# Kernel tuning notes

Measured on AMD Instinct MI355X. Metric: run time of the kernel, lower is better.

The kernel has to match this reference:

```python
import jax, jax.numpy as jnp
import numpy as np

N_HEADS = 8
HEAD_DIM = 32
MODEL_DIM = N_HEADS * HEAD_DIM  # 256
IN_DIM = 256
N_MEM = 4
B, H, W = 4, 64, 64
SCALE = HEAD_DIM ** -0.5


def setup_inputs() -> dict:
    key = jax.random.key(0)
    ks = jax.random.split(key, 6)
    x = jax.random.normal(ks[0], (B, IN_DIM, H, W), dtype=jnp.float32)
    w_qkv = jax.random.normal(ks[1], (MODEL_DIM * 3, IN_DIM), dtype=jnp.float32) * 0.02
    b_qkv = jnp.zeros((MODEL_DIM * 3,), dtype=jnp.float32)
    mem_kv = jax.random.normal(ks[2], (2, N_HEADS, N_MEM, HEAD_DIM), dtype=jnp.float32)
    w_out = jax.random.normal(ks[3], (IN_DIM, MODEL_DIM), dtype=jnp.float32) * 0.02
    b_out = jnp.zeros((IN_DIM,), dtype=jnp.float32)
    return {"x": x, "w_qkv": w_qkv, "b_qkv": b_qkv, "mem_kv": mem_kv,
            "w_out": w_out, "b_out": b_out}


def reference(x, w_qkv, b_qkv, mem_kv, w_out, b_out):
    b, c, h, w = x.shape
    n = h * w
    # 1x1 conv == per-pixel matmul over channels
    qkv = jnp.einsum('bchw,oc->bohw', x, w_qkv) + b_qkv[None, :, None, None]
    q, k, v = jnp.split(qkv, 3, axis=1)
    # 'b (n d) h w -> b n (h w) d'
    def to_heads(t):
        return t.reshape(b, N_HEADS, HEAD_DIM, n).transpose(0, 1, 3, 2)
    q, k, v = to_heads(q), to_heads(k), to_heads(v)
    # prepend memory kv tokens: [b, n_heads, N_MEM + n, d]
    mk = jnp.broadcast_to(mem_kv[0][None], (b, N_HEADS, N_MEM, HEAD_DIM))
    mv = jnp.broadcast_to(mem_kv[1][None], (b, N_HEADS, N_MEM, HEAD_DIM))
    k = jnp.concatenate([mk, k], axis=-2)
    v = jnp.concatenate([mv, v], axis=-2)
    # scaled dot-product attention (dropout prob = 0 -> identity)
    sim = jnp.einsum('bnid,bnsd->bnis', q, k) * SCALE
    attn = jax.nn.softmax(sim, axis=-1)
    out = jnp.einsum('bnis,bnsd->bnid', attn, v)
    # 'b n (h w) d -> b (n d) h w'
    out = out.transpose(0, 1, 3, 2).reshape(b, MODEL_DIM, h, w)
    out = jnp.einsum('bchw,oc->bohw', out, w_out) + b_out[None, :, None, None]
    return out
```

## Files before the change

### kernel.cpp

```cpp
#include <hip/hip_runtime.h>
#include <stdint.h>


#define DEV static __device__ __forceinline__

typedef short s16x8 __attribute__((ext_vector_type(8)));
typedef float f32x4 __attribute__((ext_vector_type(4)));
typedef unsigned short ushort_t;

DEV unsigned short f2b(float f) {
  return (unsigned short)((__float_as_uint(f) + 0x8000u) >> 16);
}
DEV unsigned pkf2b(float a, float b) {
  return __builtin_amdgcn_perm(__float_as_uint(b) + 0x8000u,
                               __float_as_uint(a) + 0x8000u, 0x07060302u);
}

DEV void gld16(const void* g, void* l) {
  __builtin_amdgcn_global_load_lds(
      (const __attribute__((address_space(1))) unsigned int*)g,
      (__attribute__((address_space(3))) unsigned int*)l, 16, 0, 0);
}

__global__ __launch_bounds__(256) void pack_x(const float* __restrict__ x,
                                              ushort_t* __restrict__ xT) {
  __shared__ float t[64][65];
  const int b = blockIdx.z, cb = blockIdx.y, pb = blockIdx.x;
  const int tid = threadIdx.x;
#pragma unroll
  for (int i = 0; i < 16; ++i) {
    int idx = i * 256 + tid;
    int cl = idx >> 6, pl = idx & 63;
    t[cl][pl] = x[((size_t)(b * 256 + cb * 64 + cl)) * 4096 + pb * 64 + pl];
  }
  __syncthreads();
#pragma unroll
  for (int i = 0; i < 8; ++i) {
    int idx = i * 256 + tid;
    int pl = idx >> 5, c2 = idx & 31;
    unsigned w = pkf2b(t[c2 * 2][pl], t[c2 * 2 + 1][pl]);
    *(unsigned*)(xT + ((size_t)(b * 4096 + pb * 64 + pl)) * 256 + cb * 64 + c2 * 2) = w;
  }
}

__global__ __launch_bounds__(256) void pack_small(
    const float* __restrict__ wqkv, const float* __restrict__ wout,
    const float* __restrict__ memkv, ushort_t* __restrict__ wqkvb,
    ushort_t* __restrict__ woutb, ushort_t* __restrict__ Kb,
    ushort_t* __restrict__ Vt) {
  int idx = blockIdx.x * 256 + threadIdx.x;
  if (idx < 196608) { wqkvb[idx] = f2b(wqkv[idx]); return; }
  idx -= 196608;
  if (idx < 65536) { woutb[idx] = f2b(wout[idx]); return; }
  idx -= 65536;
  if (idx < 131072) {
    int bh = idx >> 12, r = idx & 4095;
    int row = 4096 + (r >> 5), d = r & 31, h = bh & 7;
    float v = (row < 4100) ? memkv[h * 128 + (row - 4096) * 32 + d] : 0.f;
    Kb[((size_t)(bh * 4224 + row)) * 32 + d] = f2b(v);
    return;
  }
  idx -= 131072;
  {
    int bh = idx >> 12, r = idx & 4095;
    int d = r >> 7, col = 4096 + (r & 127), h = bh & 7;
    float v = (col < 4100) ? memkv[1024 + h * 128 + (col - 4096) * 32 + d] : 0.f;
    Vt[((size_t)(bh * 32 + d)) * 4224 + col] = f2b(v);
  }
}

__global__ __launch_bounds__(256) void qkv_gemm(
    const ushort_t* __restrict__ W, const ushort_t* __restrict__ X,
    const float* __restrict__ bias, ushort_t* __restrict__ Qb,
    ushort_t* __restrict__ Kb, ushort_t* __restrict__ Vt) {
  __shared__ ushort_t sA[128 * 32];
  __shared__ ushort_t sB[128 * 32];
  const int tid = threadIdx.x, wave = tid >> 6, lane = tid & 63;
  const int quad = lane >> 4, ln = lane & 15;
  const int b = blockIdx.z, my = blockIdx.y, nx = blockIdx.x;
  const int o0 = my * 128, p0 = nx * 128;
  const int wr = wave >> 1, wc = wave & 1;
  const ushort_t* Xb = X + (size_t)b * 4096 * 256;
  f32x4 acc[4][4];
#pragma unroll
  for (int i = 0; i < 4; ++i)
#pragma unroll
    for (int j = 0; j < 4; ++j) acc[i][j] = {0.f, 0.f, 0.f, 0.f};

  const int srow_in = lane >> 2, sgs = lane & 3;
  for (int kt = 0; kt < 8; ++kt) {
    const int k0 = kt * 32;
#pragma unroll
    for (int i2 = 0; i2 < 2; ++i2) {
      const int i = wave * 2 + i2;
      const int row = i * 16 + srow_in;
      const int gg = sgs ^ ((row >> 1) & 3);
      gld16(W + (size_t)(o0 + row) * 256 + k0 + gg * 8, sA + i * 512);
      gld16(Xb + (size_t)(p0 + row) * 256 + k0 + gg * 8, sB + i * 512);
    }
    __syncthreads();
    s16x8 af[4], bfv[4];
#pragma unroll
    for (int mt = 0; mt < 4; ++mt) {
      const int row = wr * 64 + mt * 16 + ln;
      af[mt] = *(const s16x8*)(sA + row * 32 + ((quad ^ ((row >> 1) & 3)) << 3));
    }
#pragma unroll
    for (int nt = 0; nt < 4; ++nt) {
      const int row = wc * 64 + nt * 16 + ln;
      bfv[nt] = *(const s16x8*)(sB + row * 32 + ((quad ^ ((row >> 1) & 3)) << 3));
    }
#pragma unroll
    for (int mt = 0; mt < 4; ++mt)
#pragma unroll
      for (int nt = 0; nt < 4; ++nt)
        acc[mt][nt] = __builtin_amdgcn_mfma_f32_16x16x32_bf16(af[mt], bfv[nt], acc[mt][nt], 0, 0, 0);
    __syncthreads();
  }
  const int region = o0 >> 8;
  const float qs = (region == 0) ? (0.17677669529663689f * 1.4426950408889634f) : 1.0f;
#pragma unroll
  for (int mt = 0; mt < 4; ++mt) {
    const int obase = o0 + wr * 64 + mt * 16 + quad * 4;
    const int rr = obase & 255;
    const int h = rr >> 5, d0 = rr & 31;
    const int hb = b * 8 + h;
    const float4 bv = *(const float4*)(bias + obase);
#pragma unroll
    for (int nt = 0; nt < 4; ++nt) {
      const int p_g = p0 + wc * 64 + nt * 16 + ln;
      const float v0 = (acc[mt][nt][0] + bv.x) * qs;
      const float v1 = (acc[mt][nt][1] + bv.y) * qs;
      const float v2 = (acc[mt][nt][2] + bv.z) * qs;
      const float v3 = (acc[mt][nt][3] + bv.w) * qs;
      if (region == 0) {
        *(uint2*)(Qb + ((size_t)(hb * 4096 + p_g)) * 32 + d0) =
            make_uint2(pkf2b(v0, v1), pkf2b(v2, v3));
      } else if (region == 1) {
        *(uint2*)(Kb + ((size_t)(hb * 4224 + p_g)) * 32 + d0) =
            make_uint2(pkf2b(v0, v1), pkf2b(v2, v3));
      } else {
        Vt[((size_t)(hb * 32 + d0 + 0)) * 4224 + p_g] = f2b(v0);
        Vt[((size_t)(hb * 32 + d0 + 1)) * 4224 + p_g] = f2b(v1);
        Vt[((size_t)(hb * 32 + d0 + 2)) * 4224 + p_g] = f2b(v2);
        Vt[((size_t)(hb * 32 + d0 + 3)) * 4224 + p_g] = f2b(v3);
      }
    }
  }
}

__global__ __launch_bounds__(256, 8) void flash_attn(
    const ushort_t* __restrict__ Qb, const ushort_t* __restrict__ Kb,
    const ushort_t* __restrict__ Vt, ushort_t* __restrict__ AO) {
  __shared__ ushort_t sK[128 * 32];
  __shared__ ushort_t sV[32 * 128];
  const int tid = threadIdx.x, wave = tid >> 6, lane = tid & 63;
  const int quad = lane >> 4, ln = lane & 15;
  const int bh = blockIdx.y, b = bh >> 3, h = bh & 7;
  const int q0 = blockIdx.x * 64 + wave * 16;

  const s16x8 qf = *(const s16x8*)(Qb + ((size_t)(bh * 4096 + q0 + ln)) * 32 + quad * 8);
  f32x4 acc0 = {0.f, 0.f, 0.f, 0.f}, acc1 = {0.f, 0.f, 0.f, 0.f};
  f32x4 ls4 = {0.f, 0.f, 0.f, 0.f};
  ushort_t* myP = sK + wave * 1024;
  const int krow_in = lane >> 2, kgs = lane & 3;
  const int vrow_in = lane >> 4, vgs = lane & 15;

  for (int it = 0; it < 33; ++it) {
    const int kb = it << 7;
#pragma unroll
    for (int i2 = 0; i2 < 2; ++i2) {
      const int i = wave * 2 + i2;
      {
        const int row = i * 16 + krow_in;
        const int gg = kgs ^ ((row >> 1) & 3);
        gld16(Kb + ((size_t)(bh * 4224 + kb + row)) * 32 + gg * 8, sK + i * 512);
      }
      {
        const int d = i * 4 + vrow_in;
        const int gg = vgs ^ (d & 7);
        gld16(Vt + ((size_t)(bh * 32 + d)) * 4224 + kb + gg * 8, sV + i * 512);
      }
    }
    __syncthreads();
    unsigned pk[8][2];
#pragma unroll
    for (int t = 0; t < 8; ++t) {
      const int srow = t * 16 + ln;
      s16x8 kf = *(const s16x8*)(sK + srow * 32 + ((quad ^ ((srow >> 1) & 3)) << 3));
      f32x4 z = {0.f, 0.f, 0.f, 0.f};
      f32x4 s = __builtin_amdgcn_mfma_f32_16x16x32_bf16(kf, qf, z, 0, 0, 0);
      f32x4 p;
#pragma unroll
      for (int r = 0; r < 4; ++r) p[r] = __builtin_amdgcn_exp2f(s[r]);
      if (it == 32) {
        if (!(t == 0 && quad == 0)) { p[0] = 0.f; p[1] = 0.f; p[2] = 0.f; p[3] = 0.f; }
      }
      ls4 += p;
      pk[t][0] = pkf2b(p[0], p[1]);
      pk[t][1] = pkf2b(p[2], p[3]);
    }
    __syncthreads();
#pragma unroll
    for (int h2 = 0; h2 < 2; ++h2) {
#pragma unroll
      for (int tt = 0; tt < 4; ++tt) {
        const int t = h2 * 4 + tt;
        const int off = ln * 64 + (((2 * tt + (quad >> 1)) ^ (ln & 7)) << 3) + ((quad & 1) << 2);
        *(uint2*)(myP + off) = make_uint2(pk[t][0], pk[t][1]);
      }
#pragma unroll
      for (int c = 0; c < 2; ++c) {
        const int cg = h2 * 2 + c;
        s16x8 pf = *(const s16x8*)(myP + ln * 64 + (((4 * c + quad) ^ (ln & 7)) << 3));
#pragma unroll
        for (int hh = 0; hh < 2; ++hh) {
          const int d = hh * 16 + ln;
          s16x8 vf = *(const s16x8*)(sV + d * 128 + (((cg * 4 + quad) ^ (d & 7)) << 3));
          if (hh == 0) acc0 = __builtin_amdgcn_mfma_f32_16x16x32_bf16(vf, pf, acc0, 0, 0, 0);
          else         acc1 = __builtin_amdgcn_mfma_f32_16x16x32_bf16(vf, pf, acc1, 0, 0, 0);
        }
      }
    }
    __syncthreads();
  }
  float lsum = (ls4[0] + ls4[1]) + (ls4[2] + ls4[3]);
  lsum += __shfl_xor(lsum, 16, 64);
  lsum += __shfl_xor(lsum, 32, 64);
  const float inv = 1.0f / lsum;
  ushort_t* dst = AO + ((size_t)(b * 4096 + q0 + ln)) * 256 + h * 32 + quad * 4;
  *(uint2*)(dst) = make_uint2(pkf2b(acc0[0] * inv, acc0[1] * inv),
                              pkf2b(acc0[2] * inv, acc0[3] * inv));
  *(uint2*)(dst + 16) = make_uint2(pkf2b(acc1[0] * inv, acc1[1] * inv),
                                   pkf2b(acc1[2] * inv, acc1[3] * inv));
}

__global__ __launch_bounds__(256) void out_gemm(
    const ushort_t* __restrict__ W, const ushort_t* __restrict__ A,
    const float* __restrict__ bias, float* __restrict__ Out) {
  __shared__ ushort_t sA[128 * 32];
  __shared__ ushort_t sB[128 * 32];
  const int tid = threadIdx.x, wave = tid >> 6, lane = tid & 63;
  const int quad = lane >> 4, ln = lane & 15;
  const int b = blockIdx.z, my = blockIdx.y, nx = blockIdx.x;
  const int o0 = my * 128, p0 = nx * 128;
  const int wr = wave >> 1, wc = wave & 1;
  const ushort_t* Ab = A + (size_t)b * 4096 * 256;
  f32x4 acc[4][4];
#pragma unroll
  for (int i = 0; i < 4; ++i)
#pragma unroll
    for (int j = 0; j < 4; ++j) acc[i][j] = {0.f, 0.f, 0.f, 0.f};

  const int srow_in = lane >> 2, sgs = lane & 3;
  for (int kt = 0; kt < 8; ++kt) {
    const int k0 = kt * 32;
#pragma unroll
    for (int i2 = 0; i2 < 2; ++i2) {
      const int i = wave * 2 + i2;
      const int row = i * 16 + srow_in;
      const int gg = sgs ^ ((row >> 1) & 3);
      gld16(W + (size_t)(o0 + row) * 256 + k0 + gg * 8, sA + i * 512);
      gld16(Ab + (size_t)(p0 + row) * 256 + k0 + gg * 8, sB + i * 512);
    }
    __syncthreads();
    s16x8 af[4], bfv[4];
#pragma unroll
    for (int mt = 0; mt < 4; ++mt) {
      const int row = wr * 64 + mt * 16 + ln;
      af[mt] = *(const s16x8*)(sA + row * 32 + ((quad ^ ((row >> 1) & 3)) << 3));
    }
#pragma unroll
    for (int nt = 0; nt < 4; ++nt) {
      const int row = wc * 64 + nt * 16 + ln;
      bfv[nt] = *(const s16x8*)(sB + row * 32 + ((quad ^ ((row >> 1) & 3)) << 3));
    }
#pragma unroll
    for (int mt = 0; mt < 4; ++mt)
#pragma unroll
      for (int nt = 0; nt < 4; ++nt)
        acc[mt][nt] = __builtin_amdgcn_mfma_f32_16x16x32_bf16(af[mt], bfv[nt], acc[mt][nt], 0, 0, 0);
    __syncthreads();
  }
#pragma unroll
  for (int mt = 0; mt < 4; ++mt) {
#pragma unroll
    for (int r = 0; r < 4; ++r) {
      const int o_g = o0 + wr * 64 + mt * 16 + quad * 4 + r;
      const float bv = bias[o_g];
#pragma unroll
      for (int nt = 0; nt < 4; ++nt) {
        const int p_g = p0 + wc * 64 + nt * 16 + ln;
        Out[((size_t)(b * 256 + o_g)) * 4096 + p_g] = acc[mt][nt][r] + bv;
      }
    }
  }
}

extern "C" void kernel_launch(void* const* d_in, const int* in_sizes, int n_in,
                              void* d_out, int out_size, void* d_ws, size_t ws_size,
                              hipStream_t stream) {
  (void)in_sizes; (void)n_in; (void)out_size; (void)ws_size;
  const float* x      = (const float*)d_in[0];
  const float* w_qkv  = (const float*)d_in[1];
  const float* b_qkv  = (const float*)d_in[2];
  const float* mem_kv = (const float*)d_in[3];
  const float* w_out  = (const float*)d_in[4];
  const float* b_out  = (const float*)d_in[5];
  char* ws = (char*)d_ws;
  ushort_t* xT     = (ushort_t*)(ws);
  ushort_t* wqkvb  = (ushort_t*)(ws + 8388608);
  ushort_t* woutb  = (ushort_t*)(ws + 8781824);
  ushort_t* Qb     = (ushort_t*)(ws + 8912896);
  ushort_t* Kb     = (ushort_t*)(ws + 17301504);
  ushort_t* Vt     = (ushort_t*)(ws + 25952256);
  ushort_t* AO     = (ushort_t*)(ws + 34603008);
  float* out = (float*)d_out;

  pack_x<<<dim3(64, 4, 4), 256, 0, stream>>>(x, xT);
  pack_small<<<dim3(2048), 256, 0, stream>>>(w_qkv, w_out, mem_kv, wqkvb, woutb, Kb, Vt);
  qkv_gemm<<<dim3(32, 6, 4), 256, 0, stream>>>(wqkvb, xT, b_qkv, Qb, Kb, Vt);
  flash_attn<<<dim3(64, 32), 256, 0, stream>>>(Qb, Kb, Vt, AO);
  out_gemm<<<dim3(32, 2, 4), 256, 0, stream>>>(woutb, AO, b_out, out);
}
```

Measured before the change: 241.7 us.

## Double-buffer flash attention with 32x32 MFMA and register-resident probabilities

Rewrites the attention kernel to use 32x32x16 bf16 MFMA tiles with 32 queries per wave and 128 per block. K/V tiles are double-buffered in LDS so the next tile loads while the current one computes, which removes one of the barriers per iteration. V is stored with a permuted token order in the QKV GEMM, so the exp'd scores can feed the PV MFMA straight from registers instead of taking an LDS round trip. The grid is flattened with a head-interleaved block order. The cost is more LDS and VGPRs per block (occupancy hint drops from 8 to 4), plus a correctness dependency on the V permutation matching the MFMA layout.

```diff
diff --git a/kernel.cpp b/kernel.cpp
--- a/kernel.cpp
+++ b/kernel.cpp
@@ -6,6 +6,7 @@
 
 typedef short s16x8 __attribute__((ext_vector_type(8)));
 typedef float f32x4 __attribute__((ext_vector_type(4)));
+typedef float f32x16 __attribute__((ext_vector_type(16)));
 typedef unsigned short ushort_t;
 
 DEV unsigned short f2b(float f) {
@@ -140,99 +141,131 @@
         *(uint2*)(Kb + ((size_t)(hb * 4224 + p_g)) * 32 + d0) =
             make_uint2(pkf2b(v0, v1), pkf2b(v2, v3));
       } else {
-        Vt[((size_t)(hb * 32 + d0 + 0)) * 4224 + p_g] = f2b(v0);
-        Vt[((size_t)(hb * 32 + d0 + 1)) * 4224 + p_g] = f2b(v1);
-        Vt[((size_t)(hb * 32 + d0 + 2)) * 4224 + p_g] = f2b(v2);
-        Vt[((size_t)(hb * 32 + d0 + 3)) * 4224 + p_g] = f2b(v3);
+        const int ps = (p_g & ~12) | ((p_g & 4) << 1) | ((p_g & 8) >> 1);
+        Vt[((size_t)(hb * 32 + d0 + 0)) * 4224 + ps] = f2b(v0);
+        Vt[((size_t)(hb * 32 + d0 + 1)) * 4224 + ps] = f2b(v1);
+        Vt[((size_t)(hb * 32 + d0 + 2)) * 4224 + ps] = f2b(v2);
+        Vt[((size_t)(hb * 32 + d0 + 3)) * 4224 + ps] = f2b(v3);
       }
     }
   }
 }
 
-__global__ __launch_bounds__(256, 8) void flash_attn(
+DEV void fa_stage(const ushort_t* Kbase, const ushort_t* Vbase, int kb,
+                  ushort_t* sKb, ushort_t* sVb, int wave, int lane) {
+  const int kr = wave * 16 + (lane >> 2), kg = lane & 3;
+  const int vd = wave * 4 + (lane >> 4), vg = lane & 15;
+#pragma unroll
+  for (int r = 0; r < 2; ++r) {
+    const int row = r * 64 + kr;
+    gld16(Kbase + (size_t)(kb + row) * 32 + ((kg ^ (row & 3)) << 3),
+          sKb + (r * 64 + wave * 16) * 32);
+    const int d = r * 16 + vd;
+    gld16(Vbase + (size_t)d * 4224 + kb + ((vg ^ (d & 7)) << 3),
+          sVb + (r * 16 + wave * 4) * 128);
+  }
+}
+
+template <bool TAIL>
+DEV void fa_step(const ushort_t* sKb, const ushort_t* sVb, const s16x8 qf0,
+                 const s16x8 qf1, int l32, int h, f32x16& accA, f32x16& accB,
+                 f32x4& ls4) {
+  const int NT = TAIL ? 1 : 4;
+#pragma unroll
+  for (int kt = 0; kt < NT; ++kt) {
+    const ushort_t* krow = sKb + (kt * 32 + l32) * 32;
+    const int ksw = (l32 & 3);
+    s16x8 kf0 = *(const s16x8*)(krow + ((h ^ ksw) << 3));
+    s16x8 kf1 = *(const s16x8*)(krow + (((2 + h) ^ ksw) << 3));
+    f32x16 s;
+#pragma unroll
+    for (int r = 0; r < 16; ++r) s[r] = 0.f;
+    s = __builtin_amdgcn_mfma_f32_32x32x16_bf16(kf0, qf0, s, 0, 0, 0);
+    s = __builtin_amdgcn_mfma_f32_32x32x16_bf16(kf1, qf1, s, 0, 0, 0);
+    f32x16 p;
+    if (!TAIL) {
+#pragma unroll
+      for (int r = 0; r < 16; ++r) p[r] = __builtin_amdgcn_exp2f(s[r]);
+    } else {
+#pragma unroll
+      for (int r = 0; r < 16; ++r) p[r] = 0.f;
+      if (h == 0) {
+#pragma unroll
+        for (int r = 0; r < 4; ++r) p[r] = __builtin_amdgcn_exp2f(s[r]);
+      }
+    }
+#pragma unroll
+    for (int r = 0; r < 4; ++r)
+      ls4[r] += (p[r] + p[r + 4]) + (p[r + 8] + p[r + 12]);
+    const int NC = TAIL ? 1 : 2;
+#pragma unroll
+    for (int cc = 0; cc < NC; ++cc) {
+      union { unsigned u[4]; s16x8 v; } pu;
+      const int o = cc * 8;
+      pu.u[0] = pkf2b(p[o + 0], p[o + 1]);
+      pu.u[1] = pkf2b(p[o + 2], p[o + 3]);
+      pu.u[2] = pkf2b(p[o + 4], p[o + 5]);
+      pu.u[3] = pkf2b(p[o + 6], p[o + 7]);
+      const int g = 4 * kt + 2 * cc + h;
+      s16x8 vf = *(const s16x8*)(sVb + l32 * 128 + ((g ^ (l32 & 7)) << 3));
+      if (cc == 0)
+        accA = __builtin_amdgcn_mfma_f32_32x32x16_bf16(vf, pu.v, accA, 0, 0, 0);
+      else
+        accB = __builtin_amdgcn_mfma_f32_32x32x16_bf16(vf, pu.v, accB, 0, 0, 0);
+    }
+  }
+}
+
+__global__ __launch_bounds__(256, 4) void flash_attn(
     const ushort_t* __restrict__ Qb, const ushort_t* __restrict__ Kb,
     const ushort_t* __restrict__ Vt, ushort_t* __restrict__ AO) {
-  __shared__ ushort_t sK[128 * 32];
-  __shared__ ushort_t sV[32 * 128];
+  __shared__ ushort_t sK[2][128 * 32];
+  __shared__ ushort_t sV[2][32 * 128];
   const int tid = threadIdx.x, wave = tid >> 6, lane = tid & 63;
-  const int quad = lane >> 4, ln = lane & 15;
-  const int bh = blockIdx.y, b = bh >> 3, h = bh & 7;
-  const int q0 = blockIdx.x * 64 + wave * 16;
-
-  const s16x8 qf = *(const s16x8*)(Qb + ((size_t)(bh * 4096 + q0 + ln)) * 32 + quad * 8);
-  f32x4 acc0 = {0.f, 0.f, 0.f, 0.f}, acc1 = {0.f, 0.f, 0.f, 0.f};
+  const int h = lane >> 5, l32 = lane & 31;
+  const int L = blockIdx.x;
+  const int bh = (L & 7) * 4 + ((L >> 3) & 3);
+  const int qt = L >> 5;
+  const int b = bh >> 3, head = bh & 7;
+  const int q0 = qt * 128 + wave * 32;
+
+  const ushort_t* Kbase = Kb + (size_t)bh * 4224 * 32;
+  const ushort_t* Vbase = Vt + (size_t)bh * 32 * 4224;
+  const ushort_t* qp = Qb + ((size_t)(bh * 4096 + q0 + l32)) * 32;
+  const s16x8 qf0 = *(const s16x8*)(qp + h * 8);
+  const s16x8 qf1 = *(const s16x8*)(qp + 16 + h * 8);
+
+  f32x16 accA, accB;
+#pragma unroll
+  for (int r = 0; r < 16; ++r) { accA[r] = 0.f; accB[r] = 0.f; }
   f32x4 ls4 = {0.f, 0.f, 0.f, 0.f};
-  ushort_t* myP = sK + wave * 1024;
-  const int krow_in = lane >> 2, kgs = lane & 3;
-  const int vrow_in = lane >> 4, vgs = lane & 15;
-
+
+  fa_stage(Kbase, Vbase, 0, sK[0], sV[0], wave, lane);
+  __syncthreads();
   for (int it = 0; it < 33; ++it) {
-    const int kb = it << 7;
-#pragma unroll
-    for (int i2 = 0; i2 < 2; ++i2) {
-      const int i = wave * 2 + i2;
-      {
-        const int row = i * 16 + krow_in;
-        const int gg = kgs ^ ((row >> 1) & 3);
-        gld16(Kb + ((size_t)(bh * 4224 + kb + row)) * 32 + gg * 8, sK + i * 512);
-      }
-      {
-        const int d = i * 4 + vrow_in;
-        const int gg = vgs ^ (d & 7);
-        gld16(Vt + ((size_t)(bh * 32 + d)) * 4224 + kb + gg * 8, sV + i * 512);
-      }
-    }
-    __syncthreads();
-    unsigned pk[8][2];
-#pragma unroll
-    for (int t = 0; t < 8; ++t) {
-      const int srow = t * 16 + ln;
-      s16x8 kf = *(const s16x8*)(sK + srow * 32 + ((quad ^ ((srow >> 1) & 3)) << 3));
-      f32x4 z = {0.f, 0.f, 0.f, 0.f};
-      f32x4 s = __builtin_amdgcn_mfma_f32_16x16x32_bf16(kf, qf, z, 0, 0, 0);
-      f32x4 p;
-#pragma unroll
-      for (int r = 0; r < 4; ++r) p[r] = __builtin_amdgcn_exp2f(s[r]);
-      if (it == 32) {
-        if (!(t == 0 && quad == 0)) { p[0] = 0.f; p[1] = 0.f; p[2] = 0.f; p[3] = 0.f; }
-      }
-      ls4 += p;
-      pk[t][0] = pkf2b(p[0], p[1]);
-      pk[t][1] = pkf2b(p[2], p[3]);
-    }
-    __syncthreads();
-#pragma unroll
-    for (int h2 = 0; h2 < 2; ++h2) {
-#pragma unroll
-      for (int tt = 0; tt < 4; ++tt) {
-        const int t = h2 * 4 + tt;
-        const int off = ln * 64 + (((2 * tt + (quad >> 1)) ^ (ln & 7)) << 3) + ((quad & 1) << 2);
-        *(uint2*)(myP + off) = make_uint2(pk[t][0], pk[t][1]);
-      }
-#pragma unroll
-      for (int c = 0; c < 2; ++c) {
-        const int cg = h2 * 2 + c;
-        s16x8 pf = *(const s16x8*)(myP + ln * 64 + (((4 * c + quad) ^ (ln & 7)) << 3));
-#pragma unroll
-        for (int hh = 0; hh < 2; ++hh) {
-          const int d = hh * 16 + ln;
-          s16x8 vf = *(const s16x8*)(sV + d * 128 + (((cg * 4 + quad) ^ (d & 7)) << 3));
-          if (hh == 0) acc0 = __builtin_amdgcn_mfma_f32_16x16x32_bf16(vf, pf, acc0, 0, 0, 0);
-          else         acc1 = __builtin_amdgcn_mfma_f32_16x16x32_bf16(vf, pf, acc1, 0, 0, 0);
-        }
-      }
-    }
-    __syncthreads();
-  }
+    const int cur = it & 1;
+    if (it < 32)
+      fa_stage(Kbase, Vbase, (it + 1) * 128, sK[cur ^ 1], sV[cur ^ 1], wave, lane);
+    if (it < 32)
+      fa_step<false>(sK[cur], sV[cur], qf0, qf1, l32, h, accA, accB, ls4);
+    else
+      fa_step<true>(sK[cur], sV[cur], qf0, qf1, l32, h, accA, accB, ls4);
+    if (it < 32) __syncthreads();
+  }
+
   float lsum = (ls4[0] + ls4[1]) + (ls4[2] + ls4[3]);
-  lsum += __shfl_xor(lsum, 16, 64);
   lsum += __shfl_xor(lsum, 32, 64);
   const float inv = 1.0f / lsum;
-  ushort_t* dst = AO + ((size_t)(b * 4096 + q0 + ln)) * 256 + h * 32 + quad * 4;
-  *(uint2*)(dst) = make_uint2(pkf2b(acc0[0] * inv, acc0[1] * inv),
-                              pkf2b(acc0[2] * inv, acc0[3] * inv));
-  *(uint2*)(dst + 16) = make_uint2(pkf2b(acc1[0] * inv, acc1[1] * inv),
-                                   pkf2b(acc1[2] * inv, acc1[3] * inv));
+  ushort_t* dst = AO + ((size_t)(b * 4096 + q0 + l32)) * 256 + head * 32;
+#pragma unroll
+  for (int run = 0; run < 4; ++run) {
+    const int d0 = run * 8 + 4 * h;
+    const float v0 = (accA[run * 4 + 0] + accB[run * 4 + 0]) * inv;
+    const float v1 = (accA[run * 4 + 1] + accB[run * 4 + 1]) * inv;
+    const float v2 = (accA[run * 4 + 2] + accB[run * 4 + 2]) * inv;
+    const float v3 = (accA[run * 4 + 3] + accB[run * 4 + 3]) * inv;
+    *(uint2*)(dst + d0) = make_uint2(pkf2b(v0, v1), pkf2b(v2, v3));
+  }
 }
 
 __global__ __launch_bounds__(256) void out_gemm(
@@ -320,6 +353,6 @@
   pack_x<<<dim3(64, 4, 4), 256, 0, stream>>>(x, xT);
   pack_small<<<dim3(2048), 256, 0, stream>>>(w_qkv, w_out, mem_kv, wqkvb, woutb, Kb, Vt);
   qkv_gemm<<<dim3(32, 6, 4), 256, 0, stream>>>(wqkvb, xT, b_qkv, Qb, Kb, Vt);
-  flash_attn<<<dim3(64, 32), 256, 0, stream>>>(Qb, Kb, Vt, AO);
+  flash_attn<<<dim3(1024), 256, 0, stream>>>(Qb, Kb, Vt, AO);
   out_gemm<<<dim3(32, 2, 4), 256, 0, stream>>>(woutb, AO, b_out, out);
 }
```

Result: faster. 229.8 us (-4.9%).
